# Performance work log

Measured on AMD Instinct MI355X. Metric: run time of the kernel, lower is better.

Reference implementation:

```python
import jax, jax.numpy as jnp
import numpy as np

HIDDEN = 128

def setup_inputs() -> dict:
    key = jax.random.key(0)
    ks = jax.random.split(key, 4)
    B, T, D, H = 64, 2048, 64, HIDDEN
    scale_ih = 1.0 / np.sqrt(D)
    scale_hh = 1.0 / np.sqrt(H)
    return {
        "input_data": jax.random.normal(ks[0], (B, T, D), dtype=jnp.float32),
        "W_ih": jax.random.normal(ks[1], (4 * H, D), dtype=jnp.float32) * scale_ih,
        "W_hh": jax.random.normal(ks[2], (4 * H, H), dtype=jnp.float32) * scale_hh,
        "b_ih": jnp.zeros((4 * H,), dtype=jnp.float32),
        "b_hh": jnp.zeros((4 * H,), dtype=jnp.float32),
        "h0": jnp.zeros((B, H), dtype=jnp.float32),
        "c0": jnp.zeros((B, H), dtype=jnp.float32),
    }

def reference(input_data, W_ih, W_hh, b_ih, b_hh, h0, c0):
    # Single-layer LSTM over the sequence, PyTorch gate order (i, f, g, o).
    H = h0.shape[-1]
    b = b_ih + b_hh  # (4H,)
    # Precompute input projections for all timesteps: (T, B, 4H)
    x_proj = jnp.einsum('btd,gd->tbg', input_data, W_ih) + b

    def step(carry, xp_t):
        h, c = carry  # (B, H) each
        gates = xp_t + h @ W_hh.T  # (B, 4H)
        i = jax.nn.sigmoid(gates[:, 0 * H:1 * H])
        f = jax.nn.sigmoid(gates[:, 1 * H:2 * H])
        g = jnp.tanh(gates[:, 2 * H:3 * H])
        o = jax.nn.sigmoid(gates[:, 3 * H:4 * H])
        c_new = f * c + i * g
        h_new = o * jnp.tanh(c_new)
        return (h_new, c_new), h_new

    (_, _), hs = jax.lax.scan(step, (h0, c0), x_proj)  # hs: (T, B, H)
    input_encoded = jnp.transpose(hs, (1, 0, 2))  # (B, T, H)
    return input_encoded
```

## Files before the change

### kernel.cpp

```cpp
#include <hip/hip_runtime.h>

typedef _Float16 half2f __attribute__((ext_vector_type(2)));

#define HID 128
#define G4  512
#define DIN 64

__device__ __forceinline__ float fdot2(half2f a, half2f b, float c) {
  return __builtin_amdgcn_fdot2(a, b, c, false);
}
__device__ __forceinline__ half2f as_h2(unsigned int u) {
  return __builtin_bit_cast(half2f, u);
}
__device__ __forceinline__ half2f mk2(float a, float b) {
  half2f r; r.x = (_Float16)a; r.y = (_Float16)b; return r;
}
__device__ __forceinline__ float sigmoidf_fast(float x) {
  return __builtin_amdgcn_rcpf(1.0f + __expf(-x));
}
__device__ __forceinline__ float tanhf_fast(float x) {
  return 2.0f * __builtin_amdgcn_rcpf(1.0f + __expf(-2.0f * x)) - 1.0f;
}
__device__ __forceinline__ float dpp_xor1_add(float x) {
  int m = __builtin_amdgcn_update_dpp(0, __builtin_bit_cast(int, x),
                                      0xB1, 0xF, 0xF, true);
  return x + __builtin_bit_cast(float, m);
}

__global__ __launch_bounds__(512, 2)
void xproj_kernel(const float* __restrict__ x, const float* __restrict__ Wih,
                  const float* __restrict__ bih, const float* __restrict__ bhh,
                  _Float16* __restrict__ xp, int nrows)
{
  const int gp   = threadIdx.x;
  const int unit = gp >> 2;
  const int gate = gp & 3;
  const int row  = gate * HID + unit;

  half2f wi[32];
  {
    const float4* wr = (const float4*)(Wih + (size_t)row * DIN);
#pragma unroll
    for (int q = 0; q < 16; q++) {
      float4 v = wr[q];
      wi[2 * q + 0] = mk2(v.x, v.y);
      wi[2 * q + 1] = mk2(v.z, v.w);
    }
  }
  const float bias = bih[row] + bhh[row];

  __shared__ __align__(16) _Float16 xin[8 * DIN];

  const int rows_per_block = (nrows + (int)gridDim.x - 1) / (int)gridDim.x;
  const int r0 = blockIdx.x * rows_per_block;
  const int r1 = (r0 + rows_per_block < nrows) ? (r0 + rows_per_block) : nrows;

  const int rsub = threadIdx.x >> 6;
  const int dd   = threadIdx.x & 63;

  float vld = 0.f;
  if (r0 + rsub < nrows) vld = x[(size_t)(r0 + rsub) * DIN + dd];

  for (int r = r0; r < r1; r += 8) {
    __syncthreads();
    xin[rsub * DIN + dd] = (_Float16)vld;
    __syncthreads();
    int rn = r + 8 + rsub;
    if (rn < nrows) vld = x[(size_t)rn * DIN + dd];

    const uint4* xi4 = (const uint4*)xin;
#pragma unroll
    for (int k = 0; k < 8; k++) {
      if (r + k >= r1) break;
      const uint4* rowp = xi4 + k * (DIN / 8);
      float a[4] = {bias, 0.f, 0.f, 0.f};
#pragma unroll
      for (int q = 0; q < 8; q++) {
        uint4 hv = rowp[q];
        a[q & 3] = fdot2(as_h2(hv.x), wi[4 * q + 0], a[q & 3]);
        a[q & 3] = fdot2(as_h2(hv.y), wi[4 * q + 1], a[q & 3]);
        a[q & 3] = fdot2(as_h2(hv.z), wi[4 * q + 2], a[q & 3]);
        a[q & 3] = fdot2(as_h2(hv.w), wi[4 * q + 3], a[q & 3]);
      }
      xp[(size_t)(r + k) * G4 + gp] = (_Float16)(a[0] + a[1] + a[2] + a[3]);
    }
  }
}

__global__ __launch_bounds__(256, 1)
void lstm_scan2(const float* __restrict__ Whh,
                const float* __restrict__ h0, const float* __restrict__ c0,
                const _Float16* __restrict__ xp,
                float* __restrict__ out, int T)
{
  const int tid = threadIdx.x;
  const int j   = tid >> 1;
  const int kq  = tid & 1;
  const int b   = blockIdx.x;

  half2f w0[32], w1[32], w2[32], w3[32];
  {
    const float4* r0 = (const float4*)(Whh + ((size_t)(0 * HID + j)) * HID + kq * 64);
    const float4* r1 = (const float4*)(Whh + ((size_t)(1 * HID + j)) * HID + kq * 64);
    const float4* r2 = (const float4*)(Whh + ((size_t)(2 * HID + j)) * HID + kq * 64);
    const float4* r3 = (const float4*)(Whh + ((size_t)(3 * HID + j)) * HID + kq * 64);
#pragma unroll
    for (int q = 0; q < 16; q++) {
      float4 v;
      v = r0[q]; w0[2 * q] = mk2(v.x, v.y); w0[2 * q + 1] = mk2(v.z, v.w);
      v = r1[q]; w1[2 * q] = mk2(v.x, v.y); w1[2 * q + 1] = mk2(v.z, v.w);
      v = r2[q]; w2[2 * q] = mk2(v.x, v.y); w2[2 * q + 1] = mk2(v.z, v.w);
      v = r3[q]; w3[2 * q] = mk2(v.x, v.y); w3[2 * q + 1] = mk2(v.z, v.w);
    }
  }

  __shared__ __align__(16) _Float16 h_sh[2][HID];

  float c = c0[(size_t)b * HID + j];
  if (kq == 0) h_sh[0][j] = (_Float16)h0[(size_t)b * HID + j];
  __syncthreads();

  const unsigned int* xp32 = (const unsigned int*)xp;
  const size_t xbase = (size_t)b * T * 256 + (size_t)j * 2 + kq;
  unsigned int xv = xp32[xbase];

  const _Float16* rb = h_sh[0];
  _Float16*       wb = h_sh[1];

  for (int t = 0; t < T; ++t) {
    unsigned int xv_next = 0;
    if (t + 1 < T) xv_next = xp32[xbase + (size_t)(t + 1) * 256];

    uint4 hv[8];
    const uint4* h4 = (const uint4*)(rb + kq * 64);
#pragma unroll
    for (int q = 0; q < 8; q++) hv[q] = h4[q];

    float a0 = 0.f, a1 = 0.f, a2 = 0.f, a3 = 0.f;
#pragma unroll
    for (int q = 0; q < 8; q++) {
      unsigned int d0 = hv[q].x, d1 = hv[q].y, d2 = hv[q].z, d3 = hv[q].w;
      a0 = fdot2(as_h2(d0), w0[4 * q + 0], a0);
      a1 = fdot2(as_h2(d0), w1[4 * q + 0], a1);
      a2 = fdot2(as_h2(d0), w2[4 * q + 0], a2);
      a3 = fdot2(as_h2(d0), w3[4 * q + 0], a3);
      a0 = fdot2(as_h2(d1), w0[4 * q + 1], a0);
      a1 = fdot2(as_h2(d1), w1[4 * q + 1], a1);
      a2 = fdot2(as_h2(d1), w2[4 * q + 1], a2);
      a3 = fdot2(as_h2(d1), w3[4 * q + 1], a3);
      a0 = fdot2(as_h2(d2), w0[4 * q + 2], a0);
      a1 = fdot2(as_h2(d2), w1[4 * q + 2], a1);
      a2 = fdot2(as_h2(d2), w2[4 * q + 2], a2);
      a3 = fdot2(as_h2(d2), w3[4 * q + 2], a3);
      a0 = fdot2(as_h2(d3), w0[4 * q + 3], a0);
      a1 = fdot2(as_h2(d3), w1[4 * q + 3], a1);
      a2 = fdot2(as_h2(d3), w2[4 * q + 3], a2);
      a3 = fdot2(as_h2(d3), w3[4 * q + 3], a3);
    }

    {
      half2f xh = as_h2(xv);
      float x0 = (float)xh.x, x1 = (float)xh.y;
      if (kq == 0) { a0 += x0; a1 += x1; }
      else         { a2 += x0; a3 += x1; }
    }

    a0 = dpp_xor1_add(a0);
    a1 = dpp_xor1_add(a1);
    a2 = dpp_xor1_add(a2);
    a3 = dpp_xor1_add(a3);

    float i  = sigmoidf_fast(a0);
    float f  = sigmoidf_fast(a1);
    float gg = tanhf_fast(a2);
    float o  = sigmoidf_fast(a3);
    c = f * c + i * gg;
    float h = o * tanhf_fast(c);

    if (kq == 0) {
      wb[j] = (_Float16)h;
      out[((size_t)b * T + t) * HID + j] = h;
    }
    __syncthreads();
    const _Float16* tmp = rb; rb = wb; wb = (_Float16*)tmp;
    xv = xv_next;
  }
}

__global__ __launch_bounds__(512, 2)
void lstm_scan_fb(const float* __restrict__ x, const float* __restrict__ Wih,
                  const float* __restrict__ Whh,
                  const float* __restrict__ bih, const float* __restrict__ bhh,
                  const float* __restrict__ h0, const float* __restrict__ c0,
                  float* __restrict__ out, int T)
{
  const int g = threadIdx.x;
  const int b = blockIdx.x;

  half2f w[64];
  {
    const float4* wr = (const float4*)(Whh + (size_t)g * HID);
#pragma unroll
    for (int q = 0; q < 32; q++) {
      float4 v = wr[q];
      w[2 * q + 0] = mk2(v.x, v.y);
      w[2 * q + 1] = mk2(v.z, v.w);
    }
  }
  half2f wi[32];
  float bias;
  {
    const float4* wr = (const float4*)(Wih + (size_t)g * DIN);
#pragma unroll
    for (int q = 0; q < 16; q++) {
      float4 v = wr[q];
      wi[2 * q + 0] = mk2(v.x, v.y);
      wi[2 * q + 1] = mk2(v.z, v.w);
    }
    bias = bih[g] + bhh[g];
  }

  __shared__ __align__(16) _Float16 h_sh[HID];
  __shared__ __align__(16) _Float16 xin[DIN];
  __shared__ float pre[G4];

  float c = 0.f;
  if (g < HID) {
    c = c0[(size_t)b * HID + g];
    h_sh[g] = (_Float16)h0[(size_t)b * HID + g];
  }
  if (g < DIN) xin[g] = (_Float16)x[((size_t)b * T) * DIN + g];
  __syncthreads();

  const bool is_tanh_gate = (g >= 2 * HID) && (g < 3 * HID);

  for (int t = 0; t < T; ++t) {
    float a[4] = {0.f, 0.f, 0.f, 0.f};
    const uint4* h4 = (const uint4*)h_sh;
#pragma unroll
    for (int q = 0; q < 16; q++) {
      uint4 hv = h4[q];
      a[q & 3] = fdot2(as_h2(hv.x), w[4 * q + 0], a[q & 3]);
      a[q & 3] = fdot2(as_h2(hv.y), w[4 * q + 1], a[q & 3]);
      a[q & 3] = fdot2(as_h2(hv.z), w[4 * q + 2], a[q & 3]);
      a[q & 3] = fdot2(as_h2(hv.w), w[4 * q + 3], a[q & 3]);
    }
    const uint4* x4 = (const uint4*)xin;
#pragma unroll
    for (int q = 0; q < 8; q++) {
      uint4 hv = x4[q];
      a[q & 3] = fdot2(as_h2(hv.x), wi[4 * q + 0], a[q & 3]);
      a[q & 3] = fdot2(as_h2(hv.y), wi[4 * q + 1], a[q & 3]);
      a[q & 3] = fdot2(as_h2(hv.z), wi[4 * q + 2], a[q & 3]);
      a[q & 3] = fdot2(as_h2(hv.w), wi[4 * q + 3], a[q & 3]);
    }
    float preact = a[0] + a[1] + a[2] + a[3] + bias;
    float act = is_tanh_gate ? tanhf_fast(preact) : sigmoidf_fast(preact);
    pre[g] = act;
    __syncthreads();

    if (g < HID) {
      float i  = pre[g];
      float f  = pre[g + HID];
      float gg = pre[g + 2 * HID];
      float o  = pre[g + 3 * HID];
      c = f * c + i * gg;
      float h = o * tanhf_fast(c);
      out[((size_t)b * T + t) * HID + g] = h;
      h_sh[g] = (_Float16)h;
    } else if (g >= HID && g < HID + DIN) {
      int d = g - HID;
      if (t + 1 < T) xin[d] = (_Float16)x[((size_t)b * T + (t + 1)) * DIN + d];
    }
    __syncthreads();
  }
}

extern "C" void kernel_launch(void* const* d_in, const int* in_sizes, int n_in,
                              void* d_out, int out_size, void* d_ws, size_t ws_size,
                              hipStream_t stream)
{
  const float* x   = (const float*)d_in[0];
  const float* Wih = (const float*)d_in[1];
  const float* Whh = (const float*)d_in[2];
  const float* bih = (const float*)d_in[3];
  const float* bhh = (const float*)d_in[4];
  const float* h0  = (const float*)d_in[5];
  const float* c0  = (const float*)d_in[6];
  float* out = (float*)d_out;

  const int B = in_sizes[5] / HID;
  const int T = in_sizes[0] / (B * DIN);
  const int nrows = B * T;

  const size_t xp_bytes = (size_t)nrows * G4 * sizeof(_Float16);
  if (ws_size >= xp_bytes) {
    _Float16* xp = (_Float16*)d_ws;
    xproj_kernel<<<1024, 512, 0, stream>>>(x, Wih, bih, bhh, xp, nrows);
    lstm_scan2<<<B, 256, 0, stream>>>(Whh, h0, c0, xp, out, T);
  } else {
    lstm_scan_fb<<<B, 512, 0, stream>>>(x, Wih, Whh, bih, bhh, h0, c0, out, T);
  }
}
```

Baseline: 1.050 ms.

## Split LSTM recurrence across four lanes per hidden unit with DPP reductions

The recurrent scan kernel now uses 512 threads per batch row, four lanes per hidden unit, instead of 256 with two lanes. Each lane does a quarter of the h·W_hh dot products. The partial sums are combined with two DPP xor-adds. Each lane then evaluates one gate activation, and the results are broadcast back via DPP quad broadcasts. This halves the serial per-step dot-product chain and spreads the transcendental work across lanes, at the cost of more threads, extra DPP ops and a barrier over more waves each step.

```diff
diff --git a/kernel.cpp b/kernel.cpp
--- a/kernel.cpp
+++ b/kernel.cpp
@@ -21,11 +21,24 @@
 __device__ __forceinline__ float tanhf_fast(float x) {
   return 2.0f * __builtin_amdgcn_rcpf(1.0f + __expf(-2.0f * x)) - 1.0f;
 }
-__device__ __forceinline__ float dpp_xor1_add(float x) {
+template <int CTRL>
+__device__ __forceinline__ float dpp_add(float x) {
   int m = __builtin_amdgcn_update_dpp(0, __builtin_bit_cast(int, x),
-                                      0xB1, 0xF, 0xF, true);
+                                      CTRL, 0xF, 0xF, true);
   return x + __builtin_bit_cast(float, m);
 }
+template <int CTRL>
+__device__ __forceinline__ float dpp_bcast(float x) {
+  int m = __builtin_amdgcn_update_dpp(0, __builtin_bit_cast(int, x),
+                                      CTRL, 0xF, 0xF, true);
+  return __builtin_bit_cast(float, m);
+}
+#define QP_XOR1 0xB1
+#define QP_XOR2 0x4E
+#define QP_B0   0x00
+#define QP_B1   0x55
+#define QP_B2   0xAA
+#define QP_B3   0xFF
 
 __global__ __launch_bounds__(512, 2)
 void xproj_kernel(const float* __restrict__ x, const float* __restrict__ Wih,
@@ -87,100 +100,104 @@
   }
 }
 
-__global__ __launch_bounds__(256, 1)
-void lstm_scan2(const float* __restrict__ Whh,
+__global__ __launch_bounds__(512, 2)
+void lstm_scan3(const float* __restrict__ Whh,
                 const float* __restrict__ h0, const float* __restrict__ c0,
                 const _Float16* __restrict__ xp,
                 float* __restrict__ out, int T)
 {
   const int tid = threadIdx.x;
-  const int j   = tid >> 1;
-  const int kq  = tid & 1;
+  const int j   = tid >> 2;
+  const int q   = tid & 3;
   const int b   = blockIdx.x;
 
-  half2f w0[32], w1[32], w2[32], w3[32];
-  {
-    const float4* r0 = (const float4*)(Whh + ((size_t)(0 * HID + j)) * HID + kq * 64);
-    const float4* r1 = (const float4*)(Whh + ((size_t)(1 * HID + j)) * HID + kq * 64);
-    const float4* r2 = (const float4*)(Whh + ((size_t)(2 * HID + j)) * HID + kq * 64);
-    const float4* r3 = (const float4*)(Whh + ((size_t)(3 * HID + j)) * HID + kq * 64);
-#pragma unroll
-    for (int q = 0; q < 16; q++) {
-      float4 v;
-      v = r0[q]; w0[2 * q] = mk2(v.x, v.y); w0[2 * q + 1] = mk2(v.z, v.w);
-      v = r1[q]; w1[2 * q] = mk2(v.x, v.y); w1[2 * q + 1] = mk2(v.z, v.w);
-      v = r2[q]; w2[2 * q] = mk2(v.x, v.y); w2[2 * q + 1] = mk2(v.z, v.w);
-      v = r3[q]; w3[2 * q] = mk2(v.x, v.y); w3[2 * q + 1] = mk2(v.z, v.w);
-    }
-  }
+  half2f w[4][16];
+#pragma unroll
+  for (int g = 0; g < 4; g++) {
+    const float4* wr = (const float4*)(Whh + (size_t)(g * HID + j) * HID + q * 32);
+#pragma unroll
+    for (int p = 0; p < 8; p++) {
+      float4 v = wr[p];
+      w[g][2 * p + 0] = mk2(v.x, v.y);
+      w[g][2 * p + 1] = mk2(v.z, v.w);
+    }
+  }
+
+  float selm[4];
+#pragma unroll
+  for (int g = 0; g < 4; g++) selm[g] = (q == g) ? 1.f : 0.f;
+  const float kk = (q == 2) ? -2.f : -1.f;
+  const float mm = (q == 2) ? 2.f : 1.f;
+  const float bb = (q == 2) ? -1.f : 0.f;
 
   __shared__ __align__(16) _Float16 h_sh[2][HID];
 
   float c = c0[(size_t)b * HID + j];
-  if (kq == 0) h_sh[0][j] = (_Float16)h0[(size_t)b * HID + j];
+  if (q == 0) h_sh[0][j] = (_Float16)h0[(size_t)b * HID + j];
   __syncthreads();
 
-  const unsigned int* xp32 = (const unsigned int*)xp;
-  const size_t xbase = (size_t)b * T * 256 + (size_t)j * 2 + kq;
-  unsigned int xv = xp32[xbase];
+  const size_t xbase = (size_t)b * T * G4 + tid;
+  float xv = (float)xp[xbase];
 
   const _Float16* rb = h_sh[0];
   _Float16*       wb = h_sh[1];
 
   for (int t = 0; t < T; ++t) {
-    unsigned int xv_next = 0;
-    if (t + 1 < T) xv_next = xp32[xbase + (size_t)(t + 1) * 256];
-
-    uint4 hv[8];
-    const uint4* h4 = (const uint4*)(rb + kq * 64);
-#pragma unroll
-    for (int q = 0; q < 8; q++) hv[q] = h4[q];
+    float xv_next = 0.f;
+    if (t + 1 < T) xv_next = (float)xp[xbase + (size_t)(t + 1) * G4];
+
+    uint4 hv[4];
+    const uint4* h4 = (const uint4*)(rb + q * 32);
+#pragma unroll
+    for (int p = 0; p < 4; p++) hv[p] = h4[p];
 
     float a0 = 0.f, a1 = 0.f, a2 = 0.f, a3 = 0.f;
 #pragma unroll
-    for (int q = 0; q < 8; q++) {
-      unsigned int d0 = hv[q].x, d1 = hv[q].y, d2 = hv[q].z, d3 = hv[q].w;
-      a0 = fdot2(as_h2(d0), w0[4 * q + 0], a0);
-      a1 = fdot2(as_h2(d0), w1[4 * q + 0], a1);
-      a2 = fdot2(as_h2(d0), w2[4 * q + 0], a2);
-      a3 = fdot2(as_h2(d0), w3[4 * q + 0], a3);
-      a0 = fdot2(as_h2(d1), w0[4 * q + 1], a0);
-      a1 = fdot2(as_h2(d1), w1[4 * q + 1], a1);
-      a2 = fdot2(as_h2(d1), w2[4 * q + 1], a2);
-      a3 = fdot2(as_h2(d1), w3[4 * q + 1], a3);
-      a0 = fdot2(as_h2(d2), w0[4 * q + 2], a0);
-      a1 = fdot2(as_h2(d2), w1[4 * q + 2], a1);
-      a2 = fdot2(as_h2(d2), w2[4 * q + 2], a2);
-      a3 = fdot2(as_h2(d2), w3[4 * q + 2], a3);
-      a0 = fdot2(as_h2(d3), w0[4 * q + 3], a0);
-      a1 = fdot2(as_h2(d3), w1[4 * q + 3], a1);
-      a2 = fdot2(as_h2(d3), w2[4 * q + 3], a2);
-      a3 = fdot2(as_h2(d3), w3[4 * q + 3], a3);
-    }
-
-    {
-      half2f xh = as_h2(xv);
-      float x0 = (float)xh.x, x1 = (float)xh.y;
-      if (kq == 0) { a0 += x0; a1 += x1; }
-      else         { a2 += x0; a3 += x1; }
-    }
-
-    a0 = dpp_xor1_add(a0);
-    a1 = dpp_xor1_add(a1);
-    a2 = dpp_xor1_add(a2);
-    a3 = dpp_xor1_add(a3);
-
-    float i  = sigmoidf_fast(a0);
-    float f  = sigmoidf_fast(a1);
-    float gg = tanhf_fast(a2);
-    float o  = sigmoidf_fast(a3);
-    c = f * c + i * gg;
-    float h = o * tanhf_fast(c);
-
-    if (kq == 0) {
-      wb[j] = (_Float16)h;
-      out[((size_t)b * T + t) * HID + j] = h;
-    }
+    for (int p = 0; p < 4; p++) {
+      unsigned int d0 = hv[p].x, d1 = hv[p].y, d2 = hv[p].z, d3 = hv[p].w;
+      a0 = fdot2(as_h2(d0), w[0][4 * p + 0], a0);
+      a1 = fdot2(as_h2(d0), w[1][4 * p + 0], a1);
+      a2 = fdot2(as_h2(d0), w[2][4 * p + 0], a2);
+      a3 = fdot2(as_h2(d0), w[3][4 * p + 0], a3);
+      a0 = fdot2(as_h2(d1), w[0][4 * p + 1], a0);
+      a1 = fdot2(as_h2(d1), w[1][4 * p + 1], a1);
+      a2 = fdot2(as_h2(d1), w[2][4 * p + 1], a2);
+      a3 = fdot2(as_h2(d1), w[3][4 * p + 1], a3);
+      a0 = fdot2(as_h2(d2), w[0][4 * p + 2], a0);
+      a1 = fdot2(as_h2(d2), w[1][4 * p + 2], a1);
+      a2 = fdot2(as_h2(d2), w[2][4 * p + 2], a2);
+      a3 = fdot2(as_h2(d2), w[3][4 * p + 2], a3);
+      a0 = fdot2(as_h2(d3), w[0][4 * p + 3], a0);
+      a1 = fdot2(as_h2(d3), w[1][4 * p + 3], a1);
+      a2 = fdot2(as_h2(d3), w[2][4 * p + 3], a2);
+      a3 = fdot2(as_h2(d3), w[3][4 * p + 3], a3);
+    }
+
+    a0 = fmaf(xv, selm[0], a0);
+    a1 = fmaf(xv, selm[1], a1);
+    a2 = fmaf(xv, selm[2], a2);
+    a3 = fmaf(xv, selm[3], a3);
+
+    a0 = dpp_add<QP_XOR1>(a0); a0 = dpp_add<QP_XOR2>(a0);
+    a1 = dpp_add<QP_XOR1>(a1); a1 = dpp_add<QP_XOR2>(a1);
+    a2 = dpp_add<QP_XOR1>(a2); a2 = dpp_add<QP_XOR2>(a2);
+    a3 = dpp_add<QP_XOR1>(a3); a3 = dpp_add<QP_XOR2>(a3);
+
+    float a01 = (q & 1) ? a1 : a0;
+    float a23 = (q & 1) ? a3 : a2;
+    float aq  = (q & 2) ? a23 : a01;
+    float act = fmaf(mm, __builtin_amdgcn_rcpf(1.0f + __expf(kk * aq)), bb);
+
+    float gi = dpp_bcast<QP_B0>(act);
+    float gf = dpp_bcast<QP_B1>(act);
+    float gg = dpp_bcast<QP_B2>(act);
+    float go = dpp_bcast<QP_B3>(act);
+
+    c = gf * c + gi * gg;
+    float h = go * tanhf_fast(c);
+
+    if (q == 0) wb[j] = (_Float16)h;
+    if (q == 1) out[((size_t)b * T + t) * HID + j] = h;
     __syncthreads();
     const _Float16* tmp = rb; rb = wb; wb = (_Float16*)tmp;
     xv = xv_next;
@@ -297,7 +314,7 @@
   if (ws_size >= xp_bytes) {
     _Float16* xp = (_Float16*)d_ws;
     xproj_kernel<<<1024, 512, 0, stream>>>(x, Wih, bih, bhh, xp, nrows);
-    lstm_scan2<<<B, 256, 0, stream>>>(Whh, h0, c0, xp, out, T);
+    lstm_scan3<<<B, 512, 0, stream>>>(Whh, h0, c0, xp, out, T);
   } else {
     lstm_scan_fb<<<B, 512, 0, stream>>>(x, Wih, Whh, bih, bhh, h0, c0, out, T);
   }
```

Result: slower. 1.628 ms (+55.1%).
